# Kernel tuning notes

Hardware: AMD Instinct MI355X
Metric: run time of the kernel (lower is better)

## Reference

```python
import jax, jax.numpy as jnp
import numpy as np

EMB = 1024
HEAD = 64
B = 4
S = 4096


def setup_inputs() -> dict:
    key = jax.random.key(0)
    ks = jax.random.split(key, 7)
    std = 1.0 / np.sqrt(EMB)
    return {
        "x": jax.random.normal(ks[0], (B, S, EMB), dtype=jnp.float32),
        "Wq": jax.random.uniform(ks[1], (EMB, HEAD), jnp.float32, -std, std),
        "bq": jax.random.uniform(ks[2], (HEAD,), jnp.float32, -std, std),
        "Wk": jax.random.uniform(ks[3], (EMB, HEAD), jnp.float32, -std, std),
        "bk": jax.random.uniform(ks[4], (HEAD,), jnp.float32, -std, std),
        "Wv": jax.random.uniform(ks[5], (EMB, HEAD), jnp.float32, -std, std),
        "bv": jax.random.uniform(ks[6], (HEAD,), jnp.float32, -std, std),
    }


def reference(x, Wq, bq, Wk, bk, Wv, bv):
    # Q, K, V: [B, S, HEAD]
    Q = x @ Wq + bq
    K = x @ Wk + bk
    V = x @ Wv + bv
    scale = 1.0 / jnp.sqrt(jnp.asarray(HEAD, dtype=Q.dtype))
    # scores: [B, S, S]
    scores = jnp.einsum("bqd,bkd->bqk", Q, K) * scale
    seq = x.shape[1]
    # original mask = tril(randn) sliced; masked_fill where mask==0 => causal
    causal = jnp.tril(jnp.ones((seq, seq), dtype=bool))
    scores = jnp.where(causal, scores, -jnp.inf)
    attn = jax.nn.softmax(scores, axis=-1)
    return jnp.einsum("bqk,bkd->bqd", attn, V)
```

## Files before the change

kernel.cpp:

```cpp
#include <hip/hip_runtime.h>
#include <stdint.h>

#define S_LEN 4096
#define EMB   1024
#define HEAD  64

typedef short bf16x8 __attribute__((ext_vector_type(8)));
typedef float f32x4  __attribute__((ext_vector_type(4)));
typedef float f32x16 __attribute__((ext_vector_type(16)));
typedef unsigned short ushort8 __attribute__((ext_vector_type(8)));

#define QSCALE 0.18033688011112042f

__device__ __forceinline__ unsigned short f2bf(float f) {
    union { float f; uint32_t u; } v; v.f = f;
    uint32_t r = v.u + 0x7fffu + ((v.u >> 16) & 1u);
    return (unsigned short)(r >> 16);
}

__device__ __forceinline__ int cvtpk_bf16(float lo, float hi_) {
    int r;
    asm("v_cvt_pk_bf16_f32 %0, %1, %2" : "=v"(r) : "v"(lo), "v"(hi_));
    return r;
}

__device__ __forceinline__ void gload_lds16(const void* g, void* l) {
    __builtin_amdgcn_global_load_lds(
        (const __attribute__((address_space(1))) void*)g,
        (__attribute__((address_space(3))) void*)l, 16, 0, 0);
}


__global__ void wprep_kernel(const float* __restrict__ Wq,
                             const float* __restrict__ Wk,
                             const float* __restrict__ Wv,
                             unsigned short* __restrict__ wt) {
    __shared__ float t[64][65];
    const int tid = threadIdx.x;
    const int m   = blockIdx.x >> 4;
    const int kcb = blockIdx.x & 15;
    const int k0  = kcb << 6;
    const float* W = (m == 0) ? Wq : (m == 1) ? Wk : Wv;
    for (int i = 0; i < 4; ++i) {
        const int k  = (tid >> 4) + i * 16;
        const int n4 = (tid & 15) << 2;
        float4 v = *(const float4*)&W[(k0 + k) * 64 + n4];
        t[k][n4 + 0] = v.x; t[k][n4 + 1] = v.y;
        t[k][n4 + 2] = v.z; t[k][n4 + 3] = v.w;
    }
    __syncthreads();
    const int n = tid >> 2, kq = (tid & 3) << 4;
    __align__(16) unsigned short u[16];
    for (int i = 0; i < 16; ++i) u[i] = f2bf(t[kq + i][n]);
    const int nimg = m * 64 + n;
    const int base = kcb * 12288 + nimg * 64;
    const int c0   = (kq >> 3) ^ (n & 7);
    const int c1   = ((kq >> 3) + 1) ^ (n & 7);
    *(int4*)&wt[base + c0 * 8] = *(int4*)&u[0];
    *(int4*)&wt[base + c1 * 8] = *(int4*)&u[8];
}

__global__ __launch_bounds__(512, 2) void qkv_kernel(
    const float* __restrict__ x, const unsigned short* __restrict__ wt,
    const float* __restrict__ bq, const float* __restrict__ bk,
    const float* __restrict__ bv,
    unsigned short* __restrict__ Qp, unsigned short* __restrict__ Kp,
    unsigned short* __restrict__ Vt) {

    __shared__ __align__(16) unsigned short xs[2][64 * 72];
    __shared__ __align__(16) unsigned short ws[2][12288];

    const int tid  = threadIdx.x;
    const int lane = tid & 63;
    const int w    = tid >> 6;
    const int wm   = w & 3;
    const int wn   = w >> 2;
    const int quad = lane >> 4;
    const int lid  = lane & 15;
    const int row0 = blockIdx.x * 64;

    f32x4 acc[6];
    for (int j = 0; j < 6; ++j) acc[j] = (f32x4){0.f, 0.f, 0.f, 0.f};

#define STAGE(BUF, KC)                                                         \
    do {                                                                       \
        {             \
            int rr = tid >> 3, c8 = (tid & 7) << 3;                            \
            const float* xp = &x[(row0 + rr) * EMB + (KC) * 64 + c8];          \
            float4 v0 = *(const float4*)xp;                                    \
            float4 v1 = *(const float4*)(xp + 4);                              \
            ushort8 u;                                                         \
            u[0] = f2bf(v0.x); u[1] = f2bf(v0.y);                              \
            u[2] = f2bf(v0.z); u[3] = f2bf(v0.w);                              \
            u[4] = f2bf(v1.x); u[5] = f2bf(v1.y);                              \
            u[6] = f2bf(v1.z); u[7] = f2bf(v1.w);                              \
            *(ushort8*)&xs[BUF][rr * 72 + c8] = u;                             \
        }                                                                      \
        {          \
            const unsigned short* gs = &wt[(KC) * 12288 + w * 1536 + lane * 8];\
            gload_lds16(gs,        &ws[BUF][w * 1536]);                        \
            gload_lds16(gs +  512, &ws[BUF][w * 1536 +  512]);                 \
            gload_lds16(gs + 1024, &ws[BUF][w * 1536 + 1024]);                 \
        }                                                                      \
    } while (0)

    STAGE(0, 0);
    __syncthreads();

    for (int kc = 0; kc < 16; ++kc) {
        const int cur = kc & 1;
        if (kc + 1 < 16) STAGE(cur ^ 1, kc + 1);
        for (int kk = 0; kk < 2; ++kk) {
            bf16x8 a = *(const bf16x8*)&xs[cur][(wm * 16 + lid) * 72 + kk * 32 + quad * 8];
            const int swz = ((((kk << 2) | quad) ^ (lid & 7)) << 3);
            for (int nt = 0; nt < 6; ++nt) {
                const int n = wn * 96 + nt * 16 + lid;
                bf16x8 bfr = *(const bf16x8*)&ws[cur][n * 64 + swz];
                acc[nt] = __builtin_amdgcn_mfma_f32_16x16x32_bf16(a, bfr, acc[nt], 0, 0, 0);
            }
        }
        __syncthreads();
    }
#undef STAGE

    for (int nt = 0; nt < 6; ++nt) {
        const int col = wn * 96 + nt * 16 + lid;
        const int mid = col >> 6;
        const int lc  = col & 63;
        const float bias = (mid == 0) ? bq[lc] : (mid == 1) ? bk[lc] : bv[lc];
        const int rb = row0 + wm * 16 + quad * 4;
        f32x4 v = acc[nt];
        if (mid < 2) {
            const int base = ((rb >> 5) << 11) + ((lc >> 3) << 8)
                           + ((rb & 31) << 3) + (lc & 7);
            unsigned short* P = (mid == 0) ? Qp : Kp;
            const float sc = (mid == 0) ? QSCALE : 1.0f;
            for (int j = 0; j < 4; ++j)
                P[base + j * 8] = f2bf((v[j] + bias) * sc);
        } else {
            const int bb = rb >> 12, s = rb & 4095;
            ushort4 u;
            u.x = f2bf(v[0] + bias); u.y = f2bf(v[1] + bias);
            u.z = f2bf(v[2] + bias); u.w = f2bf(v[3] + bias);
            *(ushort4*)&Vt[bb * 262144 + (s >> 3) * 512 + lc * 8 + (s & 7)] = u;
        }
    }
}

__global__ __launch_bounds__(512, 1) void flash_kernel(
    const unsigned short* __restrict__ Qp, const unsigned short* __restrict__ Kp,
    const unsigned short* __restrict__ Vt, float* __restrict__ out) {

    __shared__ __align__(16) float Obuf[8][32][66];
    __shared__ float lbuf[8][32];

    const int tid  = threadIdx.x;
    const int lane = tid & 63;
    const int w    = tid >> 6;
    const int hi   = lane >> 5;
    const int l5   = lane & 31;

    const int l  = blockIdx.x;
    const int x  = l & 7;
    const int b  = x & 3;
    const int p  = ((x >> 2) << 5) + (l >> 3);

    const unsigned short* Kb = &Kp[b * 262144];
    const unsigned short* Vb = &Vt[b * 262144];

    for (int half = 0; half < 2; ++half) {
        const int qt = half ? p : 127 - p;
        const int q0 = qt * 32;
        const int nt = qt + 1;

        bf16x8 qf[4];
#pragma unroll
        for (int dk = 0; dk < 4; ++dk)
            qf[dk] = *(const bf16x8*)&Qp[((b << 7) + qt) * 2048
                                         + (dk * 2 + hi) * 256 + l5 * 8];

        f32x16 O0 = {}, O1 = {};
        float ls = 0.f;

        int t = w;
        bf16x8 kf[4];
        if (t < nt) {
#pragma unroll
            for (int dk = 0; dk < 4; ++dk)
                kf[dk] = *(const bf16x8*)&Kb[t * 2048 + (dk * 2 + hi) * 256 + l5 * 8];
        }

        while (t < nt) {
            const int kt = t << 5;
            bf16x8 vf[2][2];
#pragma unroll
            for (int kc = 0; kc < 2; ++kc)
#pragma unroll
                for (int dh = 0; dh < 2; ++dh)
                    vf[dh][kc] = *(const bf16x8*)&Vb[(t * 4 + kc * 2 + hi) * 512
                                                     + (dh * 32 + l5) * 8];

            __builtin_amdgcn_s_setprio(1);
            f32x16 sa = {}, sb = {};
            sa = __builtin_amdgcn_mfma_f32_32x32x16_bf16(kf[0], qf[0], sa, 0, 0, 0);
            sb = __builtin_amdgcn_mfma_f32_32x32x16_bf16(kf[1], qf[1], sb, 0, 0, 0);
            sa = __builtin_amdgcn_mfma_f32_32x32x16_bf16(kf[2], qf[2], sa, 0, 0, 0);
            sb = __builtin_amdgcn_mfma_f32_32x32x16_bf16(kf[3], qf[3], sb, 0, 0, 0);
            __builtin_amdgcn_s_setprio(0);

            const int tn = t + 8;
            if (tn < nt) {
#pragma unroll
                for (int dk = 0; dk < 4; ++dk)
                    kf[dk] = *(const bf16x8*)&Kb[tn * 2048 + (dk * 2 + hi) * 256 + l5 * 8];
            }

            f32x16 st = sa + sb;

            if (t == nt - 1) {
#pragma unroll
                for (int rr = 0; rr < 16; ++rr) {
                    const int key = kt + (rr & 3) + 8 * (rr >> 2) + 4 * hi;
                    if (key > q0 + l5) st[rr] = -1e30f;
                }
            }

#pragma unroll
            for (int kc = 0; kc < 2; ++kc) {
                const int c8 = kc * 8;
                float ev[8];
#pragma unroll
                for (int i = 0; i < 8; ++i) ev[i] = __builtin_amdgcn_exp2f(st[c8 + i]);
                ls += ((ev[0] + ev[1]) + (ev[2] + ev[3])) +
                      ((ev[4] + ev[5]) + (ev[6] + ev[7]));
                const int p0 = cvtpk_bf16(ev[0], ev[1]);
                const int p1 = cvtpk_bf16(ev[2], ev[3]);
                const int p2 = cvtpk_bf16(ev[4], ev[5]);
                const int p3 = cvtpk_bf16(ev[6], ev[7]);
                auto s02 = __builtin_amdgcn_permlane32_swap(p0, p2, false, false);
                auto s13 = __builtin_amdgcn_permlane32_swap(p1, p3, false, false);
                union { int wd[4]; bf16x8 v; } pf;
                pf.wd[0] = s02[0]; pf.wd[1] = s13[0];
                pf.wd[2] = s02[1]; pf.wd[3] = s13[1];
                __builtin_amdgcn_s_setprio(1);
                O0 = __builtin_amdgcn_mfma_f32_32x32x16_bf16(pf.v, vf[0][kc], O0, 0, 0, 0);
                O1 = __builtin_amdgcn_mfma_f32_32x32x16_bf16(pf.v, vf[1][kc], O1, 0, 0, 0);
                __builtin_amdgcn_s_setprio(0);
            }
            t = tn;
        }

        const float lt = ls + __shfl_xor(ls, 32);
#pragma unroll
        for (int rr = 0; rr < 16; ++rr) {
            const int row = (rr & 3) + 8 * (rr >> 2) + 4 * hi;
            Obuf[w][row][l5]      = O0[rr];
            Obuf[w][row][32 + l5] = O1[rr];
        }
        if (lane < 32) lbuf[w][l5] = lt;
        __syncthreads();

        const int col = tid & 63;
        const int r0  = tid >> 6;
        for (int ii = 0; ii < 4; ++ii) {
            const int row = r0 + ii * 8;
            float o = 0.f, lsum = 0.f;
            for (int ww = 0; ww < 8; ++ww) {
                o    += Obuf[ww][row][col];
                lsum += lbuf[ww][row];
            }
            out[(b * S_LEN + q0 + row) * 64 + col] = o / lsum;
        }
        __syncthreads();
    }
}

extern "C" void kernel_launch(void* const* d_in, const int* in_sizes, int n_in,
                              void* d_out, int out_size, void* d_ws, size_t ws_size,
                              hipStream_t stream) {
    const float* x  = (const float*)d_in[0];
    const float* Wq = (const float*)d_in[1];
    const float* bq = (const float*)d_in[2];
    const float* Wk = (const float*)d_in[3];
    const float* bk = (const float*)d_in[4];
    const float* Wv = (const float*)d_in[5];
    const float* bv = (const float*)d_in[6];
    float* out = (float*)d_out;

    unsigned short* wt = (unsigned short*)d_ws;
    unsigned short* Qp = wt + 196608;
    unsigned short* Kp = Qp + 1048576;
    unsigned short* Vt = Kp + 1048576;

    hipLaunchKernelGGL(wprep_kernel, dim3(48), dim3(256), 0, stream, Wq, Wk, Wv, wt);
    hipLaunchKernelGGL(qkv_kernel, dim3(256), dim3(512), 0, stream,
                       x, wt, bq, bk, bv, Qp, Kp, Vt);
    hipLaunchKernelGGL(flash_kernel, dim3(256), dim3(512), 0, stream,
                       Qp, Kp, Vt, out);
}
```

Before: 133.0 us.

## Double flash waves to 16 per block and retile QKV GEMM to 2x3 fragments

The flash kernel now runs 1024 threads (16 waves) per block, with each wave striding over key tiles by 16 instead of 8, and the cross-wave reduction buffers grow to 16 slots. The QS product is accumulated in a single chain instead of two interleaved accumulators. In the QKV projection, each wave now computes a 32x48 tile (2 M fragments by 3 N fragments), reusing each B fragment for two MFMAs and reducing LDS reads per MFMA. The extra waves add more latency hiding but also more LDS usage for Obuf and a longer serial reduction, and the single accumulator chain introduces MFMA dependency stalls.

```diff
diff --git a/kernel.cpp b/kernel.cpp
--- a/kernel.cpp
+++ b/kernel.cpp
@@ -73,14 +73,15 @@
     const int tid  = threadIdx.x;
     const int lane = tid & 63;
     const int w    = tid >> 6;
-    const int wm   = w & 3;
-    const int wn   = w >> 2;
+    const int wm   = w & 1;
+    const int wn   = w >> 1;
     const int quad = lane >> 4;
     const int lid  = lane & 15;
     const int row0 = blockIdx.x * 64;
 
-    f32x4 acc[6];
-    for (int j = 0; j < 6; ++j) acc[j] = (f32x4){0.f, 0.f, 0.f, 0.f};
+    f32x4 acc[2][3];
+    for (int mf = 0; mf < 2; ++mf)
+        for (int nf = 0; nf < 3; ++nf) acc[mf][nf] = (f32x4){0.f, 0.f, 0.f, 0.f};
 
 #define STAGE(BUF, KC)                                                         \
     do {                                                                       \
@@ -111,48 +112,51 @@
         const int cur = kc & 1;
         if (kc + 1 < 16) STAGE(cur ^ 1, kc + 1);
         for (int kk = 0; kk < 2; ++kk) {
-            bf16x8 a = *(const bf16x8*)&xs[cur][(wm * 16 + lid) * 72 + kk * 32 + quad * 8];
+            bf16x8 a0 = *(const bf16x8*)&xs[cur][(wm * 32 + lid) * 72 + kk * 32 + quad * 8];
+            bf16x8 a1 = *(const bf16x8*)&xs[cur][(wm * 32 + 16 + lid) * 72 + kk * 32 + quad * 8];
             const int swz = ((((kk << 2) | quad) ^ (lid & 7)) << 3);
-            for (int nt = 0; nt < 6; ++nt) {
-                const int n = wn * 96 + nt * 16 + lid;
+            for (int nf = 0; nf < 3; ++nf) {
+                const int n = wn * 48 + nf * 16 + lid;
                 bf16x8 bfr = *(const bf16x8*)&ws[cur][n * 64 + swz];
-                acc[nt] = __builtin_amdgcn_mfma_f32_16x16x32_bf16(a, bfr, acc[nt], 0, 0, 0);
+                acc[0][nf] = __builtin_amdgcn_mfma_f32_16x16x32_bf16(a0, bfr, acc[0][nf], 0, 0, 0);
+                acc[1][nf] = __builtin_amdgcn_mfma_f32_16x16x32_bf16(a1, bfr, acc[1][nf], 0, 0, 0);
             }
         }
         __syncthreads();
     }
 #undef STAGE
 
-    for (int nt = 0; nt < 6; ++nt) {
-        const int col = wn * 96 + nt * 16 + lid;
-        const int mid = col >> 6;
-        const int lc  = col & 63;
-        const float bias = (mid == 0) ? bq[lc] : (mid == 1) ? bk[lc] : bv[lc];
-        const int rb = row0 + wm * 16 + quad * 4;
-        f32x4 v = acc[nt];
-        if (mid < 2) {
-            const int base = ((rb >> 5) << 11) + ((lc >> 3) << 8)
-                           + ((rb & 31) << 3) + (lc & 7);
-            unsigned short* P = (mid == 0) ? Qp : Kp;
-            const float sc = (mid == 0) ? QSCALE : 1.0f;
-            for (int j = 0; j < 4; ++j)
-                P[base + j * 8] = f2bf((v[j] + bias) * sc);
-        } else {
-            const int bb = rb >> 12, s = rb & 4095;
-            ushort4 u;
-            u.x = f2bf(v[0] + bias); u.y = f2bf(v[1] + bias);
-            u.z = f2bf(v[2] + bias); u.w = f2bf(v[3] + bias);
-            *(ushort4*)&Vt[bb * 262144 + (s >> 3) * 512 + lc * 8 + (s & 7)] = u;
-        }
-    }
-}
-
-__global__ __launch_bounds__(512, 1) void flash_kernel(
+    for (int mf = 0; mf < 2; ++mf)
+        for (int nf = 0; nf < 3; ++nf) {
+            const int col = wn * 48 + nf * 16 + lid;
+            const int mid = col >> 6;
+            const int lc  = col & 63;
+            const float bias = (mid == 0) ? bq[lc] : (mid == 1) ? bk[lc] : bv[lc];
+            const int rb = row0 + wm * 32 + mf * 16 + quad * 4;
+            f32x4 v = acc[mf][nf];
+            if (mid < 2) {
+                const int base = ((rb >> 5) << 11) + ((lc >> 3) << 8)
+                               + ((rb & 31) << 3) + (lc & 7);
+                unsigned short* P = (mid == 0) ? Qp : Kp;
+                const float sc = (mid == 0) ? QSCALE : 1.0f;
+                for (int j = 0; j < 4; ++j)
+                    P[base + j * 8] = f2bf((v[j] + bias) * sc);
+            } else {
+                const int bb = rb >> 12, s = rb & 4095;
+                ushort4 u;
+                u.x = f2bf(v[0] + bias); u.y = f2bf(v[1] + bias);
+                u.z = f2bf(v[2] + bias); u.w = f2bf(v[3] + bias);
+                *(ushort4*)&Vt[bb * 262144 + (s >> 3) * 512 + lc * 8 + (s & 7)] = u;
+            }
+        }
+}
+
+__global__ __launch_bounds__(1024, 1) void flash_kernel(
     const unsigned short* __restrict__ Qp, const unsigned short* __restrict__ Kp,
     const unsigned short* __restrict__ Vt, float* __restrict__ out) {
 
-    __shared__ __align__(16) float Obuf[8][32][66];
-    __shared__ float lbuf[8][32];
+    __shared__ __align__(16) float Obuf[16][32][66];
+    __shared__ float lbuf[16][32];
 
     const int tid  = threadIdx.x;
     const int lane = tid & 63;
@@ -201,21 +205,18 @@
                                                      + (dh * 32 + l5) * 8];
 
             __builtin_amdgcn_s_setprio(1);
-            f32x16 sa = {}, sb = {};
-            sa = __builtin_amdgcn_mfma_f32_32x32x16_bf16(kf[0], qf[0], sa, 0, 0, 0);
-            sb = __builtin_amdgcn_mfma_f32_32x32x16_bf16(kf[1], qf[1], sb, 0, 0, 0);
-            sa = __builtin_amdgcn_mfma_f32_32x32x16_bf16(kf[2], qf[2], sa, 0, 0, 0);
-            sb = __builtin_amdgcn_mfma_f32_32x32x16_bf16(kf[3], qf[3], sb, 0, 0, 0);
+            f32x16 st = {};
+#pragma unroll
+            for (int dk = 0; dk < 4; ++dk)
+                st = __builtin_amdgcn_mfma_f32_32x32x16_bf16(kf[dk], qf[dk], st, 0, 0, 0);
             __builtin_amdgcn_s_setprio(0);
 
-            const int tn = t + 8;
+            const int tn = t + 16;
             if (tn < nt) {
 #pragma unroll
                 for (int dk = 0; dk < 4; ++dk)
                     kf[dk] = *(const bf16x8*)&Kb[tn * 2048 + (dk * 2 + hi) * 256 + l5 * 8];
             }
-
-            f32x16 st = sa + sb;
 
             if (t == nt - 1) {
 #pragma unroll
@@ -262,10 +263,10 @@
 
         const int col = tid & 63;
         const int r0  = tid >> 6;
-        for (int ii = 0; ii < 4; ++ii) {
-            const int row = r0 + ii * 8;
+        for (int ii = 0; ii < 2; ++ii) {
+            const int row = r0 + ii * 16;
             float o = 0.f, lsum = 0.f;
-            for (int ww = 0; ww < 8; ++ww) {
+            for (int ww = 0; ww < 16; ++ww) {
                 o    += Obuf[ww][row][col];
                 lsum += lbuf[ww][row];
             }
@@ -295,6 +296,6 @@
     hipLaunchKernelGGL(wprep_kernel, dim3(48), dim3(256), 0, stream, Wq, Wk, Wv, wt);
     hipLaunchKernelGGL(qkv_kernel, dim3(256), dim3(512), 0, stream,
                        x, wt, bq, bk, bv, Qp, Kp, Vt);
-    hipLaunchKernelGGL(flash_kernel, dim3(256), dim3(512), 0, stream,
+    hipLaunchKernelGGL(flash_kernel, dim3(256), dim3(1024), 0, stream,
                        Qp, Kp, Vt, out);
 }
```

Measured after the change: 139.9 us. 1.05x slower.
